# Kernel optimization log

Hardware: AMD Instinct MI355X
Metric: run time of the kernel (lower is better)

## Reference

```python
import jax, jax.numpy as jnp
import numpy as np

IN_DIM = 512      # in_dim == hidden size (GRUCell(in_dim, in_dim))
CTX = 10          # context_length
BATCH = 64
SEQ = 512


def _gru_cell(x, h, Wih, Whh, bih, bhh):
    # torch.nn.GRUCell math; gate order in weights is (r, z, n)
    gi = x @ Wih.T + bih            # [B, 3H]
    gh = h @ Whh.T + bhh            # [B, 3H]
    i_r, i_z, i_n = jnp.split(gi, 3, axis=-1)
    h_r, h_z, h_n = jnp.split(gh, 3, axis=-1)
    r = jax.nn.sigmoid(i_r + h_r)
    z = jax.nn.sigmoid(i_z + h_z)
    n = jnp.tanh(i_n + r * h_n)
    return (1.0 - z) * n + z * h


def setup_inputs() -> dict:
    key = jax.random.key(0)
    ks = jax.random.split(key, 5)
    H = IN_DIM

    def xavier(k, shape):
        std = (2.0 / (shape[0] + shape[1])) ** 0.5
        return (std * jax.random.normal(k, shape)).astype(jnp.float32)

    def ortho(k, shape):
        a = jax.random.normal(k, shape)
        q, _ = jnp.linalg.qr(a)
        return q.astype(jnp.float32)

    v_in = jax.random.normal(ks[0], (BATCH, SEQ, IN_DIM), dtype=jnp.float32)
    return {
        "v_in": v_in,
        "Wih_f": xavier(ks[1], (3 * H, H)),
        "Whh_f": ortho(ks[2], (3 * H, H)),
        "bih_f": jnp.zeros((3 * H,), jnp.float32),
        "bhh_f": jnp.zeros((3 * H,), jnp.float32),
        "Wih_b": xavier(ks[3], (3 * H, H)),
        "Whh_b": ortho(ks[4], (3 * H, H)),
        "bih_b": jnp.zeros((3 * H,), jnp.float32),
        "bhh_b": jnp.zeros((3 * H,), jnp.float32),
    }


def reference(v_in, Wih_f, Whh_f, bih_f, bhh_f, Wih_b, Whh_b, bih_b, bhh_b):
    B, T, _ = v_in.shape
    x = v_in[:, :, :IN_DIM]                 # v_tr
    xs = jnp.transpose(x, (1, 0, 2))        # [T, B, H] time-major
    xr = xs[::-1]                           # reversed sequence for backward GRU
    h0 = jnp.zeros((B, IN_DIM), v_in.dtype)

    def step_f(h, xt):
        h2 = _gru_cell(xt, h, Wih_f, Whh_f, bih_f, bhh_f)
        return h2, h2

    def step_b(h, xt):
        h2 = _gru_cell(xt, h, Wih_b, Whh_b, bih_b, bhh_b)
        return h2, h2

    _, hs_f = jax.lax.scan(step_f, h0, xs)  # hs_f[t]: fwd state after x[t]
    _, hs_b = jax.lax.scan(step_b, h0, xr)  # hs_b[t]: bwd state after x[T-1-t]

    sl = slice(CTX, T - CTX)
    # h_enc[:, t-CTX] = concat(h_f(t) + x[t], h_b(t) + x[T-1-t])
    out = jnp.concatenate([hs_f[sl] + xs[sl], hs_b[sl] + xr[sl]], axis=-1)
    return jnp.transpose(out, (1, 0, 2))    # [B, T-2*CTX, 2H]
```

## Files before the change

### kernel.cpp

```cpp
#include <hip/hip_runtime.h>
#include <stdint.h>
#include <stddef.h>

#define T_SEQ 512
#define HDIM 512
#define CTXN 10
#define OUT_T (T_SEQ - 2 * CTXN)
#define GM 16
#define GC 16
#define NSLOT 8192

typedef __bf16 bf16x8 __attribute__((ext_vector_type(8)));
typedef float f32x4 __attribute__((ext_vector_type(4)));
typedef unsigned short u16x4 __attribute__((ext_vector_type(4)));
typedef unsigned short u16x8 __attribute__((ext_vector_type(8)));
typedef unsigned long long u64;

__device__ __forceinline__ unsigned short f2bf(float f) {
  union { float f; unsigned u; } v; v.f = f;
  unsigned r = v.u + 0x7FFFu + ((v.u >> 16) & 1u);
  return (unsigned short)(r >> 16);
}
__device__ __forceinline__ float bf2f(unsigned short b) {
  union { unsigned u; float f; } v; v.u = ((unsigned)b) << 16;
  return v.f;
}

__global__ void split_w(const float* __restrict__ wih_f, const float* __restrict__ wih_b,
                        const float* __restrict__ whh_f, const float* __restrict__ whh_b,
                        unsigned short* __restrict__ wih_hi, unsigned short* __restrict__ wih_lo,
                        unsigned short* __restrict__ whh_hi, unsigned short* __restrict__ whh_lo) {
  const int which = blockIdx.y;
  const float* src = which == 0 ? wih_f : which == 1 ? wih_b : which == 2 ? whh_f : whh_b;
  const size_t off = (which & 1) ? (size_t)1536 * HDIM : 0;
  unsigned short* dhi = (which < 2 ? wih_hi : whh_hi) + off;
  unsigned short* dlo = (which < 2 ? wih_lo : whh_lo) + off;
  size_t i = ((size_t)blockIdx.x * 256 + threadIdx.x) * 4;
  float4 v = *(const float4*)(src + i);
  u16x4 h, l;
  h.x = f2bf(v.x); l.x = f2bf(v.x - bf2f(h.x));
  h.y = f2bf(v.y); l.y = f2bf(v.y - bf2f(h.y));
  h.z = f2bf(v.z); l.z = f2bf(v.z - bf2f(h.z));
  h.w = f2bf(v.w); l.w = f2bf(v.w - bf2f(h.w));
  *(u16x4*)(dhi + i) = h;
  *(u16x4*)(dlo + i) = l;
}

__global__ __launch_bounds__(512)
void gru_rec(const float* __restrict__ x,
             const unsigned short* __restrict__ wih_hi, const unsigned short* __restrict__ wih_lo,
             const unsigned short* __restrict__ whh_hi, const unsigned short* __restrict__ whh_lo,
             const float* __restrict__ bih_f, const float* __restrict__ bhh_f,
             const float* __restrict__ bih_b, const float* __restrict__ bhh_b,
             float* __restrict__ out, u64* hbuf) {
  const int bx = blockIdx.x;
  const int g  = bx & 7;
  const int nb = bx >> 3;
  const int d  = g & 1;
  const int b0 = (g >> 1) * GM;
  const int tid = threadIdx.x;
  const int lane = tid & 63;
  const int wave = tid >> 6;
  const int lr = lane & 15, lq = lane >> 4;
  const int m = wave & 1;
  const int q = wave >> 1;

  __shared__ float part[2][4][3][16][17];
  __shared__ float hloc[GM][GC + 1];
  __shared__ float bi_s[3][GC], bh_s[3][GC];

  if (tid < 256) hloc[tid >> 4][tid & 15] = 0.f;
  if (tid < 48) {
    int g3 = tid >> 4, j = tid & 15;
    int row = g3 * HDIM + nb * GC + j;
    bi_s[g3][j] = (d ? bih_b : bih_f)[row];
    bh_s[g3][j] = (d ? bhh_b : bhh_f)[row];
  }

  const size_t wd = (size_t)d * 1536 * HDIM;
  const unsigned short* Whi = (m ? whh_hi : wih_hi) + wd;
  const unsigned short* Wlo = (m ? whh_lo : wih_lo) + wd;
  bf16x8 wh[3][4], wl[3][4];
#pragma unroll
  for (int g3 = 0; g3 < 3; g3++)
#pragma unroll
    for (int kc = 0; kc < 4; kc++) {
      size_t ofs = (size_t)(g3 * HDIM + nb * GC + lr) * HDIM + q * 128 + kc * 32 + lq * 8;
      wh[g3][kc] = *(const bf16x8*)(Whi + ofs);
      wl[g3][kc] = *(const bf16x8*)(Wlo + ofs);
    }

  u64* hb = hbuf + (size_t)g * 2 * NSLOT;

  const int gb  = tid & 15;
  const int gjj = (tid >> 4) & 1;
  const int gii = (tid >> 5) & 7;
  const int gj  = gjj * 8 + gii;
  const int gw  = (nb >> 3) * 2048 + (((nb >> 1) & 3) * 8 + gii) * 64 +
                  ((nb & 1) * 2 + gjj) * 16 + gb;

  for (int s = 0; s < T_SEQ; s++) {
    const int t = d ? (T_SEQ - 1 - s) : s;
    f32x4 acc[3];
    acc[0] = f32x4{0.f, 0.f, 0.f, 0.f};
    acc[1] = f32x4{0.f, 0.f, 0.f, 0.f};
    acc[2] = f32x4{0.f, 0.f, 0.f, 0.f};

    if (m == 0) {
      const float* xrow = x + ((size_t)(b0 + lr) * T_SEQ + t) * HDIM + q * 128 + lq * 8;
      float4 xa[4], xb[4];
#pragma unroll
      for (int kc = 0; kc < 4; kc++) {
        xa[kc] = *(const float4*)(xrow + kc * 32);
        xb[kc] = *(const float4*)(xrow + kc * 32 + 4);
      }
#pragma unroll
      for (int kc = 0; kc < 4; kc++) {
        float xe[8] = {xa[kc].x, xa[kc].y, xa[kc].z, xa[kc].w,
                       xb[kc].x, xb[kc].y, xb[kc].z, xb[kc].w};
        union { u16x8 u; bf16x8 b; } Ah, Al;
#pragma unroll
        for (int i = 0; i < 8; i++) {
          unsigned short hh = f2bf(xe[i]);
          Ah.u[i] = hh;
          Al.u[i] = f2bf(xe[i] - bf2f(hh));
        }
#pragma unroll
        for (int g3 = 0; g3 < 3; g3++) {
          acc[g3] = __builtin_amdgcn_mfma_f32_16x16x32_bf16(Ah.b, wh[g3][kc], acc[g3], 0, 0, 0);
          acc[g3] = __builtin_amdgcn_mfma_f32_16x16x32_bf16(Al.b, wh[g3][kc], acc[g3], 0, 0, 0);
          acc[g3] = __builtin_amdgcn_mfma_f32_16x16x32_bf16(Ah.b, wl[g3][kc], acc[g3], 0, 0, 0);
        }
      }
    } else {
      const u64* rp = hb + (size_t)(s & 1) * NSLOT + q * 2048 + lane;
      const unsigned want = (unsigned)s;
      u64 cur[4][8];
#pragma unroll
      for (int kc = 0; kc < 4; kc++)
#pragma unroll
        for (int i = 0; i < 8; i++)
          cur[kc][i] = __hip_atomic_load(rp + (kc * 8 + i) * 64,
                                         __ATOMIC_RELAXED, __HIP_MEMORY_SCOPE_AGENT);
#pragma unroll
      for (int kc = 0; kc < 4; kc++) {
        int it = 0;
        while (true) {
          bool ok = true;
#pragma unroll
          for (int i = 0; i < 8; i++) ok &= ((unsigned)(cur[kc][i] >> 32) == want);
          if (ok || ++it > (1 << 18)) break;
          __builtin_amdgcn_s_sleep(1);
#pragma unroll
          for (int i = 0; i < 8; i++)
            cur[kc][i] = __hip_atomic_load(rp + (kc * 8 + i) * 64,
                                           __ATOMIC_RELAXED, __HIP_MEMORY_SCOPE_AGENT);
        }
        union { u16x8 u; bf16x8 b; } Ah, Al;
#pragma unroll
        for (int i = 0; i < 8; i++) {
          unsigned dd = (unsigned)cur[kc][i];
          Ah.u[i] = (unsigned short)(dd >> 16);
          Al.u[i] = (unsigned short)(dd & 0xffffu);
        }
#pragma unroll
        for (int g3 = 0; g3 < 3; g3++) {
          acc[g3] = __builtin_amdgcn_mfma_f32_16x16x32_bf16(Ah.b, wh[g3][kc], acc[g3], 0, 0, 0);
          acc[g3] = __builtin_amdgcn_mfma_f32_16x16x32_bf16(Al.b, wh[g3][kc], acc[g3], 0, 0, 0);
          acc[g3] = __builtin_amdgcn_mfma_f32_16x16x32_bf16(Ah.b, wl[g3][kc], acc[g3], 0, 0, 0);
        }
      }
    }

#pragma unroll
    for (int g3 = 0; g3 < 3; g3++)
#pragma unroll
      for (int r = 0; r < 4; r++)
        part[m][q][g3][lr][lq * 4 + r] = acc[g3][r];
    __syncthreads();

    if (tid < 256) {
      const int col = nb * GC + gj;
      float ir = 0.f, iz = 0.f, inn = 0.f, hr = 0.f, hz = 0.f, hnn = 0.f;
#pragma unroll
      for (int qq = 0; qq < 4; qq++) {
        ir  += part[0][qq][0][gj][gb];
        iz  += part[0][qq][1][gj][gb];
        inn += part[0][qq][2][gj][gb];
        hr  += part[1][qq][0][gj][gb];
        hz  += part[1][qq][1][gj][gb];
        hnn += part[1][qq][2][gj][gb];
      }
      float rr = 1.f / (1.f + expf(-(ir + bi_s[0][gj] + hr + bh_s[0][gj])));
      float zz = 1.f / (1.f + expf(-(iz + bi_s[1][gj] + hz + bh_s[1][gj])));
      float nn = tanhf(inn + bi_s[2][gj] + rr * (hnn + bh_s[2][gj]));
      float hv = (1.f - zz) * nn + zz * hloc[gb][gj];
      hloc[gb][gj] = hv;
      unsigned short h16 = f2bf(hv);
      unsigned short l16 = f2bf(hv - bf2f(h16));
      u64* wr = hb + (size_t)((s + 1) & 1) * NSLOT;
      u64 wv = ((u64)(unsigned)(s + 1) << 32) |
               (u64)(((unsigned)h16 << 16) | (unsigned)l16);
      __hip_atomic_store(wr + gw, wv, __ATOMIC_RELAXED, __HIP_MEMORY_SCOPE_AGENT);
      if (s >= CTXN && s < T_SEQ - CTXN) {
        float xv = x[((size_t)(b0 + gb) * T_SEQ + t) * HDIM + col];
        out[((size_t)(b0 + gb) * OUT_T + (s - CTXN)) * 1024 + d * HDIM + col] = hv + xv;
      }
    }
    __syncthreads();
  }
}

extern "C" void kernel_launch(void* const* d_in, const int* in_sizes, int n_in,
                              void* d_out, int out_size, void* d_ws, size_t ws_size,
                              hipStream_t stream) {
  (void)in_sizes; (void)n_in; (void)out_size; (void)ws_size;
  const float* v_in  = (const float*)d_in[0];
  const float* Wih_f = (const float*)d_in[1];
  const float* Whh_f = (const float*)d_in[2];
  const float* bih_f = (const float*)d_in[3];
  const float* bhh_f = (const float*)d_in[4];
  const float* Wih_b = (const float*)d_in[5];
  const float* Whh_b = (const float*)d_in[6];
  const float* bih_b = (const float*)d_in[7];
  const float* bhh_b = (const float*)d_in[8];
  float* out = (float*)d_out;
  char* ws = (char*)d_ws;

  u64* hbuf = (u64*)ws;
  unsigned short* wih_hi = (unsigned short*)(ws + (size_t)(1 << 20));
  unsigned short* wih_lo = (unsigned short*)(ws + (size_t)(4 << 20));
  unsigned short* whh_hi = (unsigned short*)(ws + (size_t)(7 << 20));
  unsigned short* whh_lo = (unsigned short*)(ws + (size_t)(10 << 20));

  hipMemsetAsync(ws, 0, (size_t)8 * 2 * NSLOT * 8, stream);
  split_w<<<dim3(768, 4), 256, 0, stream>>>(Wih_f, Wih_b, Whh_f, Whh_b,
                                            wih_hi, wih_lo, whh_hi, whh_lo);
  gru_rec<<<256, 512, 0, stream>>>(v_in, wih_hi, wih_lo, whh_hi, whh_lo,
                                   bih_f, bhh_f, bih_b, bhh_b, out, hbuf);
}
```

Before: 2.113 ms.

## Prefetch next-step hidden state during gate epilogue and tighten GRU step barriers

Remaps waves so the upper four waves handle the recurrent matmul, and has those waves issue the next step's hidden-state atomic loads while the lower waves compute the gates, which overlaps the cross-block exchange latency with the epilogue. The polling loop now checks all 32 values at once with a wave-wide vote and has no sleep. The x residual load moves ahead of the matmul. Biases and the hidden state live in registers instead of LDS, the activations use fast exp/divide intrinsics, and __syncthreads is replaced with a custom LDS-only barrier. The risks are extra polling traffic without sleep, a much smaller iteration cap before timeout, and the accuracy of the fast transcendentals.

```diff
diff --git a/kernel.cpp b/kernel.cpp
--- a/kernel.cpp
+++ b/kernel.cpp
@@ -24,6 +24,12 @@
 __device__ __forceinline__ float bf2f(unsigned short b) {
   union { unsigned u; float f; } v; v.u = ((unsigned)b) << 16;
   return v.f;
+}
+
+__device__ __forceinline__ void lds_barrier() {
+  asm volatile("s_waitcnt lgkmcnt(0)" ::: "memory");
+  __builtin_amdgcn_s_barrier();
+  __builtin_amdgcn_sched_barrier(0);
 }
 
 __global__ void split_w(const float* __restrict__ wih_f, const float* __restrict__ wih_b,
@@ -62,20 +68,10 @@
   const int lane = tid & 63;
   const int wave = tid >> 6;
   const int lr = lane & 15, lq = lane >> 4;
-  const int m = wave & 1;
-  const int q = wave >> 1;
+  const int m = wave >> 2;
+  const int q = wave & 3;
 
   __shared__ float part[2][4][3][16][17];
-  __shared__ float hloc[GM][GC + 1];
-  __shared__ float bi_s[3][GC], bh_s[3][GC];
-
-  if (tid < 256) hloc[tid >> 4][tid & 15] = 0.f;
-  if (tid < 48) {
-    int g3 = tid >> 4, j = tid & 15;
-    int row = g3 * HDIM + nb * GC + j;
-    bi_s[g3][j] = (d ? bih_b : bih_f)[row];
-    bh_s[g3][j] = (d ? bhh_b : bhh_f)[row];
-  }
 
   const size_t wd = (size_t)d * 1536 * HDIM;
   const unsigned short* Whi = (m ? whh_hi : wih_hi) + wd;
@@ -98,6 +94,29 @@
   const int gj  = gjj * 8 + gii;
   const int gw  = (nb >> 3) * 2048 + (((nb >> 1) & 3) * 8 + gii) * 64 +
                   ((nb & 1) * 2 + gjj) * 16 + gb;
+  float hreg = 0.f;
+  float bi0 = 0.f, bi1 = 0.f, bi2 = 0.f, bh0 = 0.f, bh1 = 0.f, bh2 = 0.f;
+  if (tid < 256) {
+    const int col = nb * GC + gj;
+    bi0 = (d ? bih_b : bih_f)[col];
+    bi1 = (d ? bih_b : bih_f)[HDIM + col];
+    bi2 = (d ? bih_b : bih_f)[2 * HDIM + col];
+    bh0 = (d ? bhh_b : bhh_f)[col];
+    bh1 = (d ? bhh_b : bhh_f)[HDIM + col];
+    bh2 = (d ? bhh_b : bhh_f)[2 * HDIM + col];
+  }
+
+  u64 cur[4][8];
+  auto issue_batch = [&](int ss) {
+    const u64* rp = hb + (size_t)(ss & 1) * NSLOT + q * 2048 + lane;
+#pragma unroll
+    for (int kc = 0; kc < 4; kc++)
+#pragma unroll
+      for (int i = 0; i < 8; i++)
+        cur[kc][i] = __hip_atomic_load(rp + (kc * 8 + i) * 64,
+                                       __ATOMIC_RELAXED, __HIP_MEMORY_SCOPE_AGENT);
+  };
+  if (m == 1) issue_batch(0);
 
   for (int s = 0; s < T_SEQ; s++) {
     const int t = d ? (T_SEQ - 1 - s) : s;
@@ -105,6 +124,9 @@
     acc[0] = f32x4{0.f, 0.f, 0.f, 0.f};
     acc[1] = f32x4{0.f, 0.f, 0.f, 0.f};
     acc[2] = f32x4{0.f, 0.f, 0.f, 0.f};
+    float xv = 0.f;
+    if (tid < 256)
+      xv = x[((size_t)(b0 + gb) * T_SEQ + t) * HDIM + nb * GC + gj];
 
     if (m == 0) {
       const float* xrow = x + ((size_t)(b0 + lr) * T_SEQ + t) * HDIM + q * 128 + lq * 8;
@@ -133,29 +155,20 @@
         }
       }
     } else {
-      const u64* rp = hb + (size_t)(s & 1) * NSLOT + q * 2048 + lane;
       const unsigned want = (unsigned)s;
-      u64 cur[4][8];
-#pragma unroll
-      for (int kc = 0; kc < 4; kc++)
-#pragma unroll
-        for (int i = 0; i < 8; i++)
-          cur[kc][i] = __hip_atomic_load(rp + (kc * 8 + i) * 64,
-                                         __ATOMIC_RELAXED, __HIP_MEMORY_SCOPE_AGENT);
+      int it = 0;
+      while (true) {
+        bool ok = true;
+#pragma unroll
+        for (int kc = 0; kc < 4; kc++)
+#pragma unroll
+          for (int i = 0; i < 8; i++)
+            ok &= ((unsigned)(cur[kc][i] >> 32) == want);
+        if (__all(ok) || ++it > 4096) break;
+        issue_batch(s);
+      }
 #pragma unroll
       for (int kc = 0; kc < 4; kc++) {
-        int it = 0;
-        while (true) {
-          bool ok = true;
-#pragma unroll
-          for (int i = 0; i < 8; i++) ok &= ((unsigned)(cur[kc][i] >> 32) == want);
-          if (ok || ++it > (1 << 18)) break;
-          __builtin_amdgcn_s_sleep(1);
-#pragma unroll
-          for (int i = 0; i < 8; i++)
-            cur[kc][i] = __hip_atomic_load(rp + (kc * 8 + i) * 64,
-                                           __ATOMIC_RELAXED, __HIP_MEMORY_SCOPE_AGENT);
-        }
         union { u16x8 u; bf16x8 b; } Ah, Al;
 #pragma unroll
         for (int i = 0; i < 8; i++) {
@@ -177,10 +190,9 @@
 #pragma unroll
       for (int r = 0; r < 4; r++)
         part[m][q][g3][lr][lq * 4 + r] = acc[g3][r];
-    __syncthreads();
+    lds_barrier();
 
     if (tid < 256) {
-      const int col = nb * GC + gj;
       float ir = 0.f, iz = 0.f, inn = 0.f, hr = 0.f, hz = 0.f, hnn = 0.f;
 #pragma unroll
       for (int qq = 0; qq < 4; qq++) {
@@ -191,23 +203,29 @@
         hz  += part[1][qq][1][gj][gb];
         hnn += part[1][qq][2][gj][gb];
       }
-      float rr = 1.f / (1.f + expf(-(ir + bi_s[0][gj] + hr + bh_s[0][gj])));
-      float zz = 1.f / (1.f + expf(-(iz + bi_s[1][gj] + hz + bh_s[1][gj])));
-      float nn = tanhf(inn + bi_s[2][gj] + rr * (hnn + bh_s[2][gj]));
-      float hv = (1.f - zz) * nn + zz * hloc[gb][gj];
-      hloc[gb][gj] = hv;
+      float e1 = __expf(-(ir + bi0 + hr + bh0));
+      float rr = __fdividef(1.f, 1.f + e1);
+      float e2 = __expf(-(iz + bi1 + hz + bh1));
+      float zz = 1.f + e2;
+      float a  = inn + bi2 + rr * (hnn + bh2);
+      float e3 = __expf(-2.f * fabsf(a));
+      float nn = copysignf((1.f - e3) * __fdividef(1.f, 1.f + e3), a);
+      float sz = __fdividef(1.f, zz);
+      float hv = (1.f - sz) * nn + sz * hreg;
+      hv = nn + sz * (hreg - nn);
+      hreg = hv;
       unsigned short h16 = f2bf(hv);
       unsigned short l16 = f2bf(hv - bf2f(h16));
       u64* wr = hb + (size_t)((s + 1) & 1) * NSLOT;
       u64 wv = ((u64)(unsigned)(s + 1) << 32) |
                (u64)(((unsigned)h16 << 16) | (unsigned)l16);
       __hip_atomic_store(wr + gw, wv, __ATOMIC_RELAXED, __HIP_MEMORY_SCOPE_AGENT);
-      if (s >= CTXN && s < T_SEQ - CTXN) {
-        float xv = x[((size_t)(b0 + gb) * T_SEQ + t) * HDIM + col];
-        out[((size_t)(b0 + gb) * OUT_T + (s - CTXN)) * 1024 + d * HDIM + col] = hv + xv;
-      }
+      if (s >= CTXN && s < T_SEQ - CTXN)
+        out[((size_t)(b0 + gb) * OUT_T + (s - CTXN)) * 1024 + d * HDIM + nb * GC + gj] = hv + xv;
+    } else if (s + 1 < T_SEQ) {
+      issue_batch(s + 1);
     }
-    __syncthreads();
+    lds_barrier();
   }
 }
 
```

New measurement: 2.654 ms. 1.26x slower.
